# Kernel tuning notes

Measured on AMD Instinct MI355X. Metric: run time of the kernel, lower is better.

## Reference

```python
import jax, jax.numpy as jnp
import numpy as np

DIM = 64  # number of flow dimensions (block count)


def _masks(out_f, in_f, dim):
    # mask_d: 1 on the dim diagonal blocks; mask_o: 1 strictly below-block (lower-triangular off-diagonal)
    opd, ipd = out_f // dim, in_f // dim
    mask_d = np.zeros((out_f, in_f), np.float32)
    mask_o = np.ones((out_f, in_f), np.float32)
    for i in range(dim):
        mask_d[i * opd:(i + 1) * opd, i * ipd:(i + 1) * ipd] = 1.0
        mask_o[i * opd:(i + 1) * opd, i * ipd:] = 0.0
    return jnp.asarray(mask_d), jnp.asarray(mask_o)


def setup_inputs() -> dict:
    key = jax.random.key(0)
    k1, k2, k3, k4, k5 = jax.random.split(key, 5)
    B, F = 1024, 2048
    inputs = jax.random.normal(k1, (B, F), jnp.float32)
    # log-diagonal Jacobian blocks from a previous layer with per-dim input size 1
    grad = jax.random.normal(k2, (B, DIM, F // DIM, 1), jnp.float32)
    weight = jax.random.normal(k3, (F, F), jnp.float32) * 0.05
    diag_weight = jnp.log(jax.random.uniform(k4, (F, 1), jnp.float32, 1e-3, 1.0))
    bias = jax.random.uniform(k5, (F,), jnp.float32, -1.0, 1.0) / jnp.sqrt(jnp.float32(F))
    return {"inputs": inputs, "grad": grad, "weight": weight,
            "diag_weight": diag_weight, "bias": bias}


def reference(inputs, grad, weight, diag_weight, bias):
    out_f, in_f = weight.shape
    dim = DIM
    opd, ipd = out_f // dim, in_f // dim
    mask_d, mask_o = _masks(out_f, in_f, dim)

    # weight normalization with positive diagonal blocks
    w = jnp.exp(weight) * mask_d + weight * mask_o              # (out, in)
    wsn = jnp.sum(w * w, axis=-1, keepdims=True)                # (out, 1)
    w_n = jnp.exp(diag_weight) * w / jnp.sqrt(wsn)              # (out, in)
    wpl = diag_weight + weight - 0.5 * jnp.log(wsn)             # (out, in)

    out = inputs @ w_n.T + bias                                 # (B, out)

    # diagonal blocks of wpl, already transposed per-block: (dim, opd, ipd)
    wpl4 = wpl.reshape(dim, opd, dim, ipd)
    blocks = wpl4[jnp.arange(dim), :, jnp.arange(dim), :]

    B = inputs.shape[0]
    g = jnp.broadcast_to(blocks[None], (B, dim, opd, ipd))

    # combine with previous log-Jacobian: logsumexp over contracted axis
    grad_t = jnp.swapaxes(grad, -1, -2)                         # (B, dim, p, ipd)
    logdet = jax.nn.logsumexp(g[:, :, :, None, :] + grad_t[:, :, None, :, :], axis=-1)  # (B, dim, opd, p)
    return (out, logdet)
```

## Files before the change

### kernel.cpp

```cpp
#include <hip/hip_runtime.h>

#define F 2048
#define BATCH 1024

typedef short bf16x8 __attribute__((ext_vector_type(8)));
typedef float f32x4 __attribute__((ext_vector_type(4)));
typedef unsigned short u16x4 __attribute__((ext_vector_type(4)));

__device__ __forceinline__ unsigned short f2bf(float f) {
  unsigned u = __builtin_bit_cast(unsigned, f);
  unsigned r = (u + 0x7fffu + ((u >> 16) & 1u)) >> 16;
  return (unsigned short)r;
}

__device__ __forceinline__ void gload_lds16(const void* g, void* l) {
  __builtin_amdgcn_global_load_lds(
      (const __attribute__((address_space(1))) unsigned int*)g,
      (__attribute__((address_space(3))) unsigned int*)l,
      16, 0, 0);
}

__global__ __launch_bounds__(256) void prep_convert_kernel(
    const float* __restrict__ inputs, unsigned short* __restrict__ a_bf,
    const float* __restrict__ weight, const float* __restrict__ dw,
    unsigned short* __restrict__ w_n, float* __restrict__ exp_blocks)
{
  int bid = blockIdx.x;
  if (bid < 1024) {
    int idx = bid * 2048 + threadIdx.x * 8;
    float4 v0 = *(const float4*)(inputs + idx);
    float4 v1 = *(const float4*)(inputs + idx + 4);
    union { unsigned short s[8]; bf16x8 v; } o;
    o.s[0] = f2bf(v0.x); o.s[1] = f2bf(v0.y); o.s[2] = f2bf(v0.z); o.s[3] = f2bf(v0.w);
    o.s[4] = f2bf(v1.x); o.s[5] = f2bf(v1.y); o.s[6] = f2bf(v1.z); o.s[7] = f2bf(v1.w);
    *(bf16x8*)(a_bf + idx) = o.v;
    return;
  }
  int rb = bid - 1024;
  int lane = threadIdx.x & 63;
  int r = rb * 4 + (threadIdx.x >> 6);
  int i = r >> 5;
  int lim = (i + 1) * 32;
  int wlim = (r & ~63) + 64;
  int d0 = i * 32;
  const float* wrow = weight + (size_t)r * F;

  float ss = 0.f;
  for (int j = lane; j < lim / 4; j += 64) {
    float4 v = ((const float4*)wrow)[j];
    if (j * 4 >= d0) {
      v.x = __expf(v.x); v.y = __expf(v.y); v.z = __expf(v.z); v.w = __expf(v.w);
    }
    ss += v.x * v.x + v.y * v.y + v.z * v.z + v.w * v.w;
  }
#pragma unroll
  for (int d = 32; d > 0; d >>= 1) ss += __shfl_xor(ss, d, 64);

  float dwr = dw[r];
  float scale = __expf(dwr) * rsqrtf(ss);
  float halflog = 0.5f * __logf(ss);

  unsigned short* onrow = w_n + (size_t)r * F;
  for (int j = lane; j < wlim / 4; j += 64) {
    u16x4 o = {0, 0, 0, 0};
    if (j * 4 < lim) {
      float4 v = ((const float4*)wrow)[j];
      if (j * 4 >= d0) {
        v.x = __expf(v.x); v.y = __expf(v.y); v.z = __expf(v.z); v.w = __expf(v.w);
      }
      o[0] = f2bf(scale * v.x); o[1] = f2bf(scale * v.y);
      o[2] = f2bf(scale * v.z); o[3] = f2bf(scale * v.w);
    }
    *(u16x4*)(onrow + j * 4) = o;
  }
  if (lane < 32) {
    exp_blocks[(size_t)r * 32 + lane] = __expf(dwr + wrow[d0 + lane] - halflog);
  }
}

__global__ __launch_bounds__(256) void gemm_logdet_kernel(
    const unsigned short* __restrict__ A, const unsigned short* __restrict__ W,
    const float* __restrict__ bias, const float* __restrict__ grad,
    const float* __restrict__ exp_blocks, float* __restrict__ out,
    float* __restrict__ ld)
{
  __shared__ __align__(16) char smem[3 * 16384];

  int id = blockIdx.x;
  int tm = id >> 5;
  int tn_raw = id & 31;
  int tn = (tm & 8) ? (31 - tn_raw) : tn_raw;
  int m0 = tm * 64, n0 = tn * 64;
  int nkt = tn + 1;

  int tid = threadIdx.x;
  int lane = tid & 63, wid = tid >> 6;
  int wm = wid >> 1, wn = wid & 1;
  int l15 = lane & 15, lg = lane >> 4;

  int srow = lane >> 3;
  int schunk = (lane & 7) ^ (srow & 7);

  auto stage = [&](int buf, int kt) {
    size_t kb = (size_t)kt * 128;
    char* base = smem + buf * 16384;
#pragma unroll
    for (int e = 0; e < 2; ++e) {
      int s = wid * 2 + e;
      int row = s * 8 + srow;
      const char* ga = (const char*)A + (size_t)(m0 + row) * (F * 2) + kb + schunk * 16;
      gload_lds16(ga, base + s * 1024);
      const char* gb = (const char*)W + (size_t)(n0 + row) * (F * 2) + kb + schunk * 16;
      gload_lds16(gb, base + 8192 + s * 1024);
    }
  };

  f32x4 acc[2][2] = {};

  auto compute = [&](int buf) {
    const char* sA = smem + buf * 16384;
    const char* sB = sA + 8192;
    bf16x8 af[2][2], bfr[2][2];
#pragma unroll
    for (int mi = 0; mi < 2; ++mi)
#pragma unroll
      for (int ks = 0; ks < 2; ++ks) {
        int row = wm * 32 + mi * 16 + l15;
        int ch = (ks * 4 + lg) ^ (l15 & 7);
        af[mi][ks] = *(const bf16x8*)(sA + row * 128 + ch * 16);
      }
#pragma unroll
    for (int ni = 0; ni < 2; ++ni)
#pragma unroll
      for (int ks = 0; ks < 2; ++ks) {
        int row = wn * 32 + ni * 16 + l15;
        int ch = (ks * 4 + lg) ^ (l15 & 7);
        bfr[ni][ks] = *(const bf16x8*)(sB + row * 128 + ch * 16);
      }
#pragma unroll
    for (int ks = 0; ks < 2; ++ks)
#pragma unroll
      for (int mi = 0; mi < 2; ++mi)
#pragma unroll
        for (int ni = 0; ni < 2; ++ni)
          acc[mi][ni] = __builtin_amdgcn_mfma_f32_16x16x32_bf16(
              af[mi][ks], bfr[ni][ks], acc[mi][ni], 0, 0, 0);
  };

  stage(0, 0);
  if (nkt > 1) stage(1, 1);
  for (int kt = 0; kt < nkt; ++kt) {
    if (kt + 2 < nkt) stage((kt + 2) % 3, kt + 2);
    int rem = nkt - 1 - kt;
    if (rem >= 2)      asm volatile("s_waitcnt vmcnt(8)" ::: "memory");
    else if (rem == 1) asm volatile("s_waitcnt vmcnt(4)" ::: "memory");
    else               asm volatile("s_waitcnt vmcnt(0)" ::: "memory");
    __builtin_amdgcn_s_barrier();
    compute(kt % 3);
    __builtin_amdgcn_s_barrier();
  }

  float bv0 = bias[n0 + wn * 32 + l15];
  float bv1 = bias[n0 + wn * 32 + 16 + l15];
#pragma unroll
  for (int mi = 0; mi < 2; ++mi)
#pragma unroll
    for (int ni = 0; ni < 2; ++ni) {
      float bv = ni ? bv1 : bv0;
#pragma unroll
      for (int j = 0; j < 4; ++j) {
        int m = m0 + wm * 32 + mi * 16 + lg * 4 + j;
        int n = n0 + wn * 32 + ni * 16 + l15;
        out[(size_t)m * F + n] = acc[mi][ni][j] + bv;
      }
    }

  float* eb = (float*)smem;
  float* eg = (float*)(smem + 32 * 36 * 4);
  int li = id & 63;
  int bg0 = (id >> 6) * 4;
  int p = tid & 31, row8 = tid >> 5;

#pragma unroll
  for (int k = 0; k < 4; ++k) {
    int t = tid + k * 256;
    eb[(t >> 5) * 36 + (t & 31)] = exp_blocks[(size_t)li * 1024 + t];
  }

#pragma unroll
  for (int g4 = 0; g4 < 4; ++g4) {
    int b0 = (bg0 + g4) * 32;
    __syncthreads();
#pragma unroll
    for (int k = 0; k < 4; ++k) {
      int b = b0 + row8 + 8 * k;
      eg[(row8 + 8 * k) * 32 + p] = __expf(grad[((size_t)b * 64 + li) * 32 + p]);
    }
    __syncthreads();
    float s[4] = {0.f, 0.f, 0.f, 0.f};
#pragma unroll
    for (int q4 = 0; q4 < 8; ++q4) {
      f32x4 e = *(const f32x4*)(eb + p * 36 + q4 * 4);
#pragma unroll
      for (int k = 0; k < 4; ++k) {
        f32x4 g = *(const f32x4*)(eg + (row8 + 8 * k) * 32 + q4 * 4);
        s[k] += e[0] * g[0] + e[1] * g[1] + e[2] * g[2] + e[3] * g[3];
      }
    }
#pragma unroll
    for (int k = 0; k < 4; ++k) {
      int b = b0 + row8 + 8 * k;
      ld[((size_t)b * 64 + li) * 32 + p] = __logf(s[k]);
    }
  }
}

extern "C" void kernel_launch(void* const* d_in, const int* in_sizes, int n_in,
                              void* d_out, int out_size, void* d_ws, size_t ws_size,
                              hipStream_t stream)
{
  const float* inputs = (const float*)d_in[0];
  const float* grad   = (const float*)d_in[1];
  const float* weight = (const float*)d_in[2];
  const float* dw     = (const float*)d_in[3];
  const float* bias   = (const float*)d_in[4];

  float* out = (float*)d_out;
  float* ld  = out + (size_t)BATCH * F;

  unsigned short* w_n  = (unsigned short*)d_ws;
  unsigned short* a_bf = w_n + (size_t)F * F;
  float* exp_blocks    = (float*)(a_bf + (size_t)BATCH * F);

  prep_convert_kernel<<<1536, 256, 0, stream>>>(inputs, a_bf, weight, dw, w_n, exp_blocks);
  gemm_logdet_kernel<<<512, 256, 0, stream>>>(a_bf, w_n, bias, grad, exp_blocks, out, ld);
}
```

Before: 106.0 us.

## Pair triangular GEMM tiles per block and split logdet into MFMA blocks

Each GEMM block now handles two complementary column tiles (p and 31-p) of the block-triangular weight, so all 256 GEMM blocks do the same 33 k-tiles instead of varying amounts. The stage ring grows from three to four buffers to match. The logdet work moves out of the GEMM blocks into its own 256 blocks, which compute the exp-sum contraction with bf16 MFMA instead of scalar FP32 dot products through LDS. This aims to remove load imbalance and let the logdet work run alongside the GEMM, at the cost of bf16 rounding inside the logsumexp products and more LDS per block.

Result: faster. 99.87 us (-5.8%).

```diff
diff --git a/kernel.cpp b/kernel.cpp
--- a/kernel.cpp
+++ b/kernel.cpp
@@ -84,133 +84,164 @@
     const float* __restrict__ exp_blocks, float* __restrict__ out,
     float* __restrict__ ld)
 {
-  __shared__ __align__(16) char smem[3 * 16384];
+  __shared__ __align__(16) char smem[4 * 16384];
 
   int id = blockIdx.x;
-  int tm = id >> 5;
-  int tn_raw = id & 31;
-  int tn = (tm & 8) ? (31 - tn_raw) : tn_raw;
-  int m0 = tm * 64, n0 = tn * 64;
-  int nkt = tn + 1;
-
   int tid = threadIdx.x;
   int lane = tid & 63, wid = tid >> 6;
-  int wm = wid >> 1, wn = wid & 1;
   int l15 = lane & 15, lg = lane >> 4;
 
-  int srow = lane >> 3;
-  int schunk = (lane & 7) ^ (srow & 7);
-
-  auto stage = [&](int buf, int kt) {
-    size_t kb = (size_t)kt * 128;
-    char* base = smem + buf * 16384;
-#pragma unroll
-    for (int e = 0; e < 2; ++e) {
-      int s = wid * 2 + e;
-      int row = s * 8 + srow;
-      const char* ga = (const char*)A + (size_t)(m0 + row) * (F * 2) + kb + schunk * 16;
-      gload_lds16(ga, base + s * 1024);
-      const char* gb = (const char*)W + (size_t)(n0 + row) * (F * 2) + kb + schunk * 16;
-      gload_lds16(gb, base + 8192 + s * 1024);
-    }
-  };
-
-  f32x4 acc[2][2] = {};
-
-  auto compute = [&](int buf) {
-    const char* sA = smem + buf * 16384;
-    const char* sB = sA + 8192;
-    bf16x8 af[2][2], bfr[2][2];
-#pragma unroll
-    for (int mi = 0; mi < 2; ++mi)
-#pragma unroll
-      for (int ks = 0; ks < 2; ++ks) {
+  if (id < 256) {
+    int tm = id >> 4;
+    int p  = id & 15;
+    int m0 = tm * 64;
+    int n0a = p * 64;
+    int n0b = (31 - p) * 64;
+    int nk1 = p + 1;
+
+    int wm = wid >> 1, wn = wid & 1;
+    int srow = lane >> 3;
+    int schunk = (lane & 7) ^ (srow & 7);
+
+    auto stage = [&](int s) {
+      int n0, kt;
+      if (s < nk1) { n0 = n0a; kt = s; } else { n0 = n0b; kt = s - nk1; }
+      size_t kb = (size_t)kt * 128;
+      char* base = smem + (s & 3) * 16384;
+#pragma unroll
+      for (int e = 0; e < 2; ++e) {
+        int sg = wid * 2 + e;
+        int row = sg * 8 + srow;
+        gload_lds16((const char*)A + (size_t)(m0 + row) * 4096 + kb + schunk * 16,
+                    base + sg * 1024);
+        gload_lds16((const char*)W + (size_t)(n0 + row) * 4096 + kb + schunk * 16,
+                    base + 8192 + sg * 1024);
+      }
+    };
+
+    f32x4 acc_a[2][2] = {};
+    f32x4 acc_b[2][2] = {};
+
+    auto compute = [&](int s, f32x4 (*acc)[2]) {
+      const char* sA = smem + (s & 3) * 16384;
+      const char* sB = sA + 8192;
+      bf16x8 af[2][2], bfr[2][2];
+#pragma unroll
+      for (int mi = 0; mi < 2; ++mi) {
         int row = wm * 32 + mi * 16 + l15;
-        int ch = (ks * 4 + lg) ^ (l15 & 7);
-        af[mi][ks] = *(const bf16x8*)(sA + row * 128 + ch * 16);
-      }
-#pragma unroll
-    for (int ni = 0; ni < 2; ++ni)
-#pragma unroll
-      for (int ks = 0; ks < 2; ++ks) {
+#pragma unroll
+        for (int ks = 0; ks < 2; ++ks) {
+          int ch = (ks * 4 + lg) ^ (row & 7);
+          af[mi][ks] = *(const bf16x8*)(sA + row * 128 + ch * 16);
+        }
+      }
+#pragma unroll
+      for (int ni = 0; ni < 2; ++ni) {
         int row = wn * 32 + ni * 16 + l15;
-        int ch = (ks * 4 + lg) ^ (l15 & 7);
-        bfr[ni][ks] = *(const bf16x8*)(sB + row * 128 + ch * 16);
-      }
-#pragma unroll
-    for (int ks = 0; ks < 2; ++ks)
+#pragma unroll
+        for (int ks = 0; ks < 2; ++ks) {
+          int ch = (ks * 4 + lg) ^ (row & 7);
+          bfr[ni][ks] = *(const bf16x8*)(sB + row * 128 + ch * 16);
+        }
+      }
+#pragma unroll
+      for (int ks = 0; ks < 2; ++ks)
+#pragma unroll
+        for (int mi = 0; mi < 2; ++mi)
+#pragma unroll
+          for (int ni = 0; ni < 2; ++ni)
+            acc[mi][ni] = __builtin_amdgcn_mfma_f32_16x16x32_bf16(
+                af[mi][ks], bfr[ni][ks], acc[mi][ni], 0, 0, 0);
+    };
+
+    stage(0); stage(1); stage(2);
+    int s = 0;
+    for (; s < nk1; ++s) {
+      if (s + 3 < 33) stage(s + 3);
+      int rem = 32 - s;
+      if (rem >= 3)      asm volatile("s_waitcnt vmcnt(12)" ::: "memory");
+      else if (rem == 2) asm volatile("s_waitcnt vmcnt(8)" ::: "memory");
+      else if (rem == 1) asm volatile("s_waitcnt vmcnt(4)" ::: "memory");
+      else               asm volatile("s_waitcnt vmcnt(0)" ::: "memory");
+      __builtin_amdgcn_s_barrier();
+      compute(s, acc_a);
+      __builtin_amdgcn_s_barrier();
+    }
+    for (; s < 33; ++s) {
+      if (s + 3 < 33) stage(s + 3);
+      int rem = 32 - s;
+      if (rem >= 3)      asm volatile("s_waitcnt vmcnt(12)" ::: "memory");
+      else if (rem == 2) asm volatile("s_waitcnt vmcnt(8)" ::: "memory");
+      else if (rem == 1) asm volatile("s_waitcnt vmcnt(4)" ::: "memory");
+      else               asm volatile("s_waitcnt vmcnt(0)" ::: "memory");
+      __builtin_amdgcn_s_barrier();
+      compute(s, acc_b);
+      __builtin_amdgcn_s_barrier();
+    }
+
+#pragma unroll
+    for (int t = 0; t < 2; ++t) {
+      int n0 = t ? n0b : n0a;
+      f32x4 (*acc)[2] = t ? acc_b : acc_a;
+      float bv0 = bias[n0 + wn * 32 + l15];
+      float bv1 = bias[n0 + wn * 32 + 16 + l15];
 #pragma unroll
       for (int mi = 0; mi < 2; ++mi)
 #pragma unroll
-        for (int ni = 0; ni < 2; ++ni)
-          acc[mi][ni] = __builtin_amdgcn_mfma_f32_16x16x32_bf16(
-              af[mi][ks], bfr[ni][ks], acc[mi][ni], 0, 0, 0);
-  };
-
-  stage(0, 0);
-  if (nkt > 1) stage(1, 1);
-  for (int kt = 0; kt < nkt; ++kt) {
-    if (kt + 2 < nkt) stage((kt + 2) % 3, kt + 2);
-    int rem = nkt - 1 - kt;
-    if (rem >= 2)      asm volatile("s_waitcnt vmcnt(8)" ::: "memory");
-    else if (rem == 1) asm volatile("s_waitcnt vmcnt(4)" ::: "memory");
-    else               asm volatile("s_waitcnt vmcnt(0)" ::: "memory");
-    __builtin_amdgcn_s_barrier();
-    compute(kt % 3);
-    __builtin_amdgcn_s_barrier();
-  }
-
-  float bv0 = bias[n0 + wn * 32 + l15];
-  float bv1 = bias[n0 + wn * 32 + 16 + l15];
-#pragma unroll
-  for (int mi = 0; mi < 2; ++mi)
-#pragma unroll
-    for (int ni = 0; ni < 2; ++ni) {
-      float bv = ni ? bv1 : bv0;
+        for (int ni = 0; ni < 2; ++ni) {
+          float bv = ni ? bv1 : bv0;
+#pragma unroll
+          for (int j = 0; j < 4; ++j) {
+            int m = m0 + wm * 32 + mi * 16 + lg * 4 + j;
+            int n = n0 + wn * 32 + ni * 16 + l15;
+            out[(size_t)m * F + n] = acc[mi][ni][j] + bv;
+          }
+        }
+    }
+  } else {
+    int lid = id - 256;
+    int i = lid & 63;
+    int bq = lid >> 6;
+    int b_base = bq * 256 + wid * 64;
+
+    const float* ebp = exp_blocks + (size_t)i * 1024;
+    bf16x8 eb_lo, eb_hi;
+    {
+      float4 a0 = *(const float4*)(ebp + l15 * 32 + lg * 8);
+      float4 a1 = *(const float4*)(ebp + l15 * 32 + lg * 8 + 4);
+      float4 b0 = *(const float4*)(ebp + (16 + l15) * 32 + lg * 8);
+      float4 b1 = *(const float4*)(ebp + (16 + l15) * 32 + lg * 8 + 4);
+      union { unsigned short s[8]; bf16x8 v; } plo, phi;
+      plo.s[0] = f2bf(a0.x); plo.s[1] = f2bf(a0.y); plo.s[2] = f2bf(a0.z); plo.s[3] = f2bf(a0.w);
+      plo.s[4] = f2bf(a1.x); plo.s[5] = f2bf(a1.y); plo.s[6] = f2bf(a1.z); plo.s[7] = f2bf(a1.w);
+      phi.s[0] = f2bf(b0.x); phi.s[1] = f2bf(b0.y); phi.s[2] = f2bf(b0.z); phi.s[3] = f2bf(b0.w);
+      phi.s[4] = f2bf(b1.x); phi.s[5] = f2bf(b1.y); phi.s[6] = f2bf(b1.z); phi.s[7] = f2bf(b1.w);
+      eb_lo = plo.v; eb_hi = phi.v;
+    }
+
+    const f32x4 zero = {0.f, 0.f, 0.f, 0.f};
+#pragma unroll
+    for (int g = 0; g < 4; ++g) {
+      int brow = b_base + g * 16 + l15;
+      const float* gp = grad + (size_t)brow * 2048 + i * 32 + lg * 8;
+      float4 g0 = *(const float4*)gp;
+      float4 g1 = *(const float4*)(gp + 4);
+      union { unsigned short s[8]; bf16x8 v; } pg;
+      pg.s[0] = f2bf(__expf(g0.x)); pg.s[1] = f2bf(__expf(g0.y));
+      pg.s[2] = f2bf(__expf(g0.z)); pg.s[3] = f2bf(__expf(g0.w));
+      pg.s[4] = f2bf(__expf(g1.x)); pg.s[5] = f2bf(__expf(g1.y));
+      pg.s[6] = f2bf(__expf(g1.z)); pg.s[7] = f2bf(__expf(g1.w));
+
+      f32x4 dlo = __builtin_amdgcn_mfma_f32_16x16x32_bf16(pg.v, eb_lo, zero, 0, 0, 0);
+      f32x4 dhi = __builtin_amdgcn_mfma_f32_16x16x32_bf16(pg.v, eb_hi, zero, 0, 0, 0);
+
 #pragma unroll
       for (int j = 0; j < 4; ++j) {
-        int m = m0 + wm * 32 + mi * 16 + lg * 4 + j;
-        int n = n0 + wn * 32 + ni * 16 + l15;
-        out[(size_t)m * F + n] = acc[mi][ni][j] + bv;
-      }
-    }
-
-  float* eb = (float*)smem;
-  float* eg = (float*)(smem + 32 * 36 * 4);
-  int li = id & 63;
-  int bg0 = (id >> 6) * 4;
-  int p = tid & 31, row8 = tid >> 5;
-
-#pragma unroll
-  for (int k = 0; k < 4; ++k) {
-    int t = tid + k * 256;
-    eb[(t >> 5) * 36 + (t & 31)] = exp_blocks[(size_t)li * 1024 + t];
-  }
-
-#pragma unroll
-  for (int g4 = 0; g4 < 4; ++g4) {
-    int b0 = (bg0 + g4) * 32;
-    __syncthreads();
-#pragma unroll
-    for (int k = 0; k < 4; ++k) {
-      int b = b0 + row8 + 8 * k;
-      eg[(row8 + 8 * k) * 32 + p] = __expf(grad[((size_t)b * 64 + li) * 32 + p]);
-    }
-    __syncthreads();
-    float s[4] = {0.f, 0.f, 0.f, 0.f};
-#pragma unroll
-    for (int q4 = 0; q4 < 8; ++q4) {
-      f32x4 e = *(const f32x4*)(eb + p * 36 + q4 * 4);
-#pragma unroll
-      for (int k = 0; k < 4; ++k) {
-        f32x4 g = *(const f32x4*)(eg + (row8 + 8 * k) * 32 + q4 * 4);
-        s[k] += e[0] * g[0] + e[1] * g[1] + e[2] * g[2] + e[3] * g[3];
-      }
-    }
-#pragma unroll
-    for (int k = 0; k < 4; ++k) {
-      int b = b0 + row8 + 8 * k;
-      ld[((size_t)b * 64 + li) * 32 + p] = __logf(s[k]);
+        int bb = b_base + g * 16 + lg * 4 + j;
+        float* dst = ld + ((size_t)bb * 64 + i) * 32;
+        dst[l15] = __logf(dlo[j]);
+        dst[16 + l15] = __logf(dhi[j]);
+      }
     }
   }
 }
```
